# Performance work log

Measured on AMD Instinct MI355X. Metric: run time of the kernel, lower is better.

## Reference

```python
import jax, jax.numpy as jnp
import numpy as np

V = 8192        # num_embeddings == n_nodes
E = 262144      # n_edges (avg degree 32)
N = 262144      # lookup batch
D = 128         # out_channels
LAMDA = 0.8
EPS = 1e-12


def setup_inputs() -> dict:
    key = jax.random.key(0)
    k0, k1, k2, k3, k4 = jax.random.split(key, 5)
    x = jax.random.randint(k0, (N,), 0, V)
    edge_index = jax.random.randint(k1, (2, E), 0, V)
    edge_weight = jax.random.uniform(k2, (E,), dtype=jnp.float32)
    embedding = jax.random.normal(k3, (V, V), dtype=jnp.float32) * 0.02
    W = jax.random.normal(k4, (V, D), dtype=jnp.float32) * (1.0 / np.sqrt(V))
    b = jnp.zeros((D,), dtype=jnp.float32)
    return {"x": x, "edge_index": edge_index, "edge_weight": edge_weight,
            "embedding": embedding, "W": W, "b": b}


def reference(x, edge_index, edge_weight, embedding, W, b):
    # Embedding_sim: linear transform then sparse adjacency propagation
    H = embedding @ W + b                       # [V, D]
    src, dst = edge_index[0], edge_index[1]
    msg = H[src] * edge_weight[:, None]         # gather + weight, [E, D]
    P = jax.ops.segment_sum(msg, dst, num_segments=V)  # spmm(A, H), [V, D]
    emb = LAMDA * P + (1.0 - LAMDA) * H         # [V, D]
    # dropout is identity in eval mode
    out = emb[x]                                # embedding lookup, [N, D]
    norm = jnp.linalg.norm(out, axis=-1, keepdims=True)
    return out / jnp.maximum(norm, EPS)         # F.normalize (L2, dim=1)
```

## Files before the change

kernel.cpp:

```cpp
#include <hip/hip_runtime.h>
#include <hip/hip_bf16.h>

#define V     8192
#define E_N   262144
#define NN    262144
#define D     128
#define KDIM  8192

typedef __attribute__((ext_vector_type(8))) short b16x8;
typedef __attribute__((ext_vector_type(4))) float f32x4;

static __device__ __forceinline__ unsigned short f2bf(float f) {
    union { float f; unsigned int u; } v; v.f = f;
    unsigned int r = v.u + 0x7FFFu + ((v.u >> 16) & 1u);
    return (unsigned short)(r >> 16);
}

static __device__ __forceinline__ unsigned int cvtpk(float lo, float hi) {
    unsigned int r;
    asm("v_cvt_pk_bf16_f32 %0, %1, %2" : "=v"(r) : "v"(lo), "v"(hi));
    return r;
}

__global__ void k_pack(const float* __restrict__ W, unsigned short* __restrict__ Wp) {
    __shared__ float tile[32][129];
    int kb = blockIdx.x;
    int t  = threadIdx.x;
    #pragma unroll
    for (int i = 0; i < 16; i++) {
        int lin = i * 256 + t;
        int kk = lin >> 7, c = lin & 127;
        tile[kk][c] = W[(size_t)(kb * 32 + kk) * D + c];
    }
    __syncthreads();
    unsigned short* outp = Wp + (size_t)kb * 4096;
    #pragma unroll
    for (int i = 0; i < 16; i++) {
        int o = i * 256 + t;
        int c = o >> 5, kk = o & 31;
        outp[o] = f2bf(tile[kk][c]);
    }
}

__global__ void k_initH(float* __restrict__ H, const float* __restrict__ b) {
    int t = blockIdx.x * 256 + threadIdx.x;
    H[t] = b[t & (D - 1)];
}

__global__ void k_hist(const int* __restrict__ dst, int* __restrict__ hist) {
    int e = blockIdx.x * 256 + threadIdx.x;
    if (e < E_N) atomicAdd(&hist[dst[e]], 1);
}

__global__ void k_scan(const int* __restrict__ hist, int* __restrict__ offsets,
                       int* __restrict__ cursor) {
    __shared__ int part[1024];
    int t = threadIdx.x;
    int base = t * 8;
    int loc[8]; int s = 0;
    for (int i = 0; i < 8; i++) { loc[i] = s; s += hist[base + i]; }
    part[t] = s;
    __syncthreads();
    for (int st = 1; st < 1024; st <<= 1) {
        int v = (t >= st) ? part[t - st] : 0;
        __syncthreads();
        part[t] += v;
        __syncthreads();
    }
    int ex = (t == 0) ? 0 : part[t - 1];
    for (int i = 0; i < 8; i++) {
        int o = ex + loc[i];
        offsets[base + i] = o;
        cursor[base + i] = o;
    }
    if (t == 1023) offsets[8192] = ex + s;
}

__global__ void k_scatter(const int* __restrict__ srcI, const int* __restrict__ dstI,
                          const float* __restrict__ w, int* __restrict__ cursor,
                          int* __restrict__ src_s, float* __restrict__ w_s) {
    int e = blockIdx.x * 256 + threadIdx.x;
    if (e < E_N) {
        int dnode = dstI[e];
        int pos = atomicAdd(&cursor[dnode], 1);
        src_s[pos] = srcI[e];
        w_s[pos]  = w[e];
    }
}

__global__ void __launch_bounds__(256) k_gemm(const float* __restrict__ A,
                                              const unsigned short* __restrict__ Wp,
                                              float* __restrict__ H) {
    const int rb   = blockIdx.x >> 3;
    const int ks   = blockIdx.x & 7;
    const int tid  = threadIdx.x;
    const int w    = tid >> 6;
    const int lane = tid & 63;
    const int r16  = lane & 15;
    const int kg   = lane >> 4;

    const float* aP = A + (size_t)(rb * 64 + w * 16 + r16) * KDIM + ks * 1024 + kg * 8;
    const unsigned short* bP = Wp + (size_t)(ks * 32) * 4096 + r16 * 32 + kg * 8;

    f32x4 acc[8];
    f32x4 zero = {0.f, 0.f, 0.f, 0.f};
    #pragma unroll
    for (int t = 0; t < 8; t++) acc[t] = zero;

#define ISSUE(aa0, aa1, bb, kt)                                        \
    do {                                                               \
        const float* ap_ = aP + (kt) * 32;                             \
        aa0 = *(const f32x4*)ap_;                                      \
        aa1 = *(const f32x4*)(ap_ + 4);                                \
        const b16x8* bp_ = (const b16x8*)(bP + (size_t)(kt) * 4096);   \
        _Pragma("unroll")                                              \
        for (int t = 0; t < 8; t++) bb[t] = bp_[t * 64];               \
    } while (0)

#define COMPUTE(aa0, aa1, bb)                                                          \
    do {                                                                               \
        union { b16x8 v; unsigned int u[4]; } af_;                                     \
        af_.u[0] = cvtpk(aa0[0], aa0[1]);                                              \
        af_.u[1] = cvtpk(aa0[2], aa0[3]);                                              \
        af_.u[2] = cvtpk(aa1[0], aa1[1]);                                              \
        af_.u[3] = cvtpk(aa1[2], aa1[3]);                                              \
        _Pragma("unroll")                                                              \
        for (int t = 0; t < 8; t++)                                                    \
            acc[t] = __builtin_amdgcn_mfma_f32_16x16x32_bf16(af_.v, bb[t], acc[t], 0, 0, 0); \
    } while (0)

    f32x4 a0A, a1A, a0B, a1B;
    b16x8 bA[8], bB[8];

    ISSUE(a0A, a1A, bA, 0);
    for (int kt = 0; kt < 32; kt += 2) {
        ISSUE(a0B, a1B, bB, kt + 1);
        COMPUTE(a0A, a1A, bA);
        ISSUE(a0A, a1A, bA, (kt + 2) & 31);
        COMPUTE(a0B, a1B, bB);
    }
#undef ISSUE
#undef COMPUTE

    const int rbase = rb * 64 + w * 16 + kg * 4;
    #pragma unroll
    for (int t = 0; t < 8; t++) {
        int col = t * 16 + r16;
        #pragma unroll
        for (int j = 0; j < 4; j++)
            atomicAdd(&H[(size_t)(rbase + j) * D + col], acc[t][j]);
    }
}

__global__ void k_emb(const float* __restrict__ H, const int* __restrict__ offsets,
                      const int* __restrict__ src_s, const float* __restrict__ w_s,
                      float* __restrict__ embn) {
    __shared__ float red[128];
    int v = blockIdx.x;
    int d = threadIdx.x;
    int s0 = offsets[v], s1 = offsets[v + 1];
    float acc = 0.f;
    for (int i = s0; i < s1; i++) {
        int s = src_s[i];
        float w = w_s[i];
        acc = fmaf(w, H[(size_t)s * D + d], acc);
    }
    float e = 0.8f * acc + 0.2f * H[(size_t)v * D + d];
    red[d] = e * e;
    __syncthreads();
    for (int st = 64; st > 0; st >>= 1) {
        if (d < st) red[d] += red[d + st];
        __syncthreads();
    }
    float norm = sqrtf(red[0]);
    float scale = 1.f / fmaxf(norm, 1e-12f);
    embn[(size_t)v * D + d] = e * scale;
}

__global__ void k_out(const int* __restrict__ x, const float* __restrict__ embn,
                      float* __restrict__ out) {
    int t = blockIdx.x * 256 + threadIdx.x;
    int n = t >> 5, c = t & 31;
    int xv = x[n];
    ((f32x4*)out)[t] = ((const f32x4*)embn)[xv * 32 + c];
}

extern "C" void kernel_launch(void* const* d_in, const int* in_sizes, int n_in,
                              void* d_out, int out_size, void* d_ws, size_t ws_size,
                              hipStream_t stream) {
    const int*   x      = (const int*)d_in[0];
    const int*   eSrc   = (const int*)d_in[1];
    const int*   eDst   = ((const int*)d_in[1]) + E_N;
    const float* eW     = (const float*)d_in[2];
    const float* A      = (const float*)d_in[3];
    const float* W      = (const float*)d_in[4];
    const float* b      = (const float*)d_in[5];
    float* out = (float*)d_out;

    char* ws = (char*)d_ws;
    unsigned short* Wp  = (unsigned short*)(ws);
    float* H            = (float*)(ws + (2u << 20));
    float* embn         = (float*)(ws + (6u << 20));
    int* offsets        = (int*)(ws + (10u << 20));
    int* cursor         = (int*)(ws + (10u << 20) + 40960);
    int* src_s          = (int*)(ws + (10u << 20) + 131072);
    float* w_s          = (float*)(ws + (10u << 20) + 131072 + (1u << 20));

    hipMemsetAsync(cursor, 0, V * sizeof(int), stream);
    k_pack   <<<256, 256, 0, stream>>>(W, Wp);
    k_initH  <<<(V * D) / 256, 256, 0, stream>>>(H, b);
    k_hist   <<<E_N / 256, 256, 0, stream>>>(eDst, cursor);
    k_scan   <<<1, 1024, 0, stream>>>(cursor, offsets, cursor);
    k_scatter<<<E_N / 256, 256, 0, stream>>>(eSrc, eDst, eW, cursor, src_s, w_s);
    k_gemm   <<<1024, 256, 0, stream>>>(A, Wp, H);
    k_emb    <<<V, D, 0, stream>>>(H, offsets, src_s, w_s, embn);
    k_out    <<<(NN * 32) / 256, 256, 0, stream>>>(x, embn, out);
}
```

Baseline: 227.3 us.

## Replace split-K atomics with partial buffers and deepen GEMM prefetch pipeline

The GEMM now splits K four ways instead of eight, uses 512 blocks, and writes each split's partial results to its own buffer instead of doing float atomicAdd into H. A new combine kernel sums the four partials and adds the bias, which also removes the separate bias-init kernel. The cursor memset is folded into the pack kernel, and the GEMM main loop keeps four A stages and two B stages in flight with a launch-bounds occupancy hint. This trades global atomic traffic and two launches for extra partial-buffer memory traffic, one extra launch, and fewer blocks to hide latency.

```diff
diff --git a/kernel.cpp b/kernel.cpp
--- a/kernel.cpp
+++ b/kernel.cpp
@@ -22,10 +22,12 @@
     return r;
 }
 
-__global__ void k_pack(const float* __restrict__ W, unsigned short* __restrict__ Wp) {
+__global__ void k_pack(const float* __restrict__ W, unsigned short* __restrict__ Wp,
+                       int* __restrict__ cursor) {
     __shared__ float tile[32][129];
     int kb = blockIdx.x;
     int t  = threadIdx.x;
+    if (kb < 32) cursor[kb * 256 + t] = 0;
     #pragma unroll
     for (int i = 0; i < 16; i++) {
         int lin = i * 256 + t;
@@ -40,11 +42,6 @@
         int c = o >> 5, kk = o & 31;
         outp[o] = f2bf(tile[kk][c]);
     }
-}
-
-__global__ void k_initH(float* __restrict__ H, const float* __restrict__ b) {
-    int t = blockIdx.x * 256 + threadIdx.x;
-    H[t] = b[t & (D - 1)];
 }
 
 __global__ void k_hist(const int* __restrict__ dst, int* __restrict__ hist) {
@@ -88,68 +85,81 @@
     }
 }
 
-__global__ void __launch_bounds__(256) k_gemm(const float* __restrict__ A,
-                                              const unsigned short* __restrict__ Wp,
-                                              float* __restrict__ H) {
-    const int rb   = blockIdx.x >> 3;
-    const int ks   = blockIdx.x & 7;
+__global__ void __launch_bounds__(256, 2) k_gemm(const float* __restrict__ A,
+                                                 const unsigned short* __restrict__ Wp,
+                                                 float* __restrict__ Hp) {
+    const int rb   = blockIdx.x >> 2;
+    const int ks   = blockIdx.x & 3;
     const int tid  = threadIdx.x;
     const int w    = tid >> 6;
     const int lane = tid & 63;
     const int r16  = lane & 15;
     const int kg   = lane >> 4;
 
-    const float* aP = A + (size_t)(rb * 64 + w * 16 + r16) * KDIM + ks * 1024 + kg * 8;
-    const unsigned short* bP = Wp + (size_t)(ks * 32) * 4096 + r16 * 32 + kg * 8;
+    const float* aP = A + (size_t)(rb * 64 + w * 16 + r16) * KDIM + ks * 2048 + kg * 8;
+    const unsigned short* bP = Wp + (size_t)(ks * 64) * 4096 + r16 * 32 + kg * 8;
 
     f32x4 acc[8];
     f32x4 zero = {0.f, 0.f, 0.f, 0.f};
     #pragma unroll
     for (int t = 0; t < 8; t++) acc[t] = zero;
 
-#define ISSUE(aa0, aa1, bb, kt)                                        \
-    do {                                                               \
-        const float* ap_ = aP + (kt) * 32;                             \
-        aa0 = *(const f32x4*)ap_;                                      \
-        aa1 = *(const f32x4*)(ap_ + 4);                                \
-        const b16x8* bp_ = (const b16x8*)(bP + (size_t)(kt) * 4096);   \
-        _Pragma("unroll")                                              \
-        for (int t = 0; t < 8; t++) bb[t] = bp_[t * 64];               \
+#define LDA(s0, s1, p)                                                  \
+    do { const float* ap_ = aP + (size_t)(p) * 32;                      \
+         s0 = *(const f32x4*)ap_; s1 = *(const f32x4*)(ap_ + 4); } while (0)
+#define LDB(bb, p)                                                      \
+    do { const b16x8* bp_ = (const b16x8*)(bP + (size_t)(p) * 4096);    \
+         _Pragma("unroll")                                              \
+         for (int t = 0; t < 8; t++) bb[t] = bp_[t * 64]; } while (0)
+#define COMP(s0, s1, bb)                                                \
+    do { union { b16x8 v; unsigned int u[4]; } af_;                     \
+         af_.u[0] = cvtpk(s0[0], s0[1]);                                \
+         af_.u[1] = cvtpk(s0[2], s0[3]);                                \
+         af_.u[2] = cvtpk(s1[0], s1[1]);                                \
+         af_.u[3] = cvtpk(s1[2], s1[3]);                                \
+         _Pragma("unroll")                                              \
+         for (int t = 0; t < 8; t++)                                    \
+             acc[t] = __builtin_amdgcn_mfma_f32_16x16x32_bf16(af_.v, bb[t], acc[t], 0, 0, 0); \
     } while (0)
-
-#define COMPUTE(aa0, aa1, bb)                                                          \
-    do {                                                                               \
-        union { b16x8 v; unsigned int u[4]; } af_;                                     \
-        af_.u[0] = cvtpk(aa0[0], aa0[1]);                                              \
-        af_.u[1] = cvtpk(aa0[2], aa0[3]);                                              \
-        af_.u[2] = cvtpk(aa1[0], aa1[1]);                                              \
-        af_.u[3] = cvtpk(aa1[2], aa1[3]);                                              \
-        _Pragma("unroll")                                                              \
-        for (int t = 0; t < 8; t++)                                                    \
-            acc[t] = __builtin_amdgcn_mfma_f32_16x16x32_bf16(af_.v, bb[t], acc[t], 0, 0, 0); \
-    } while (0)
-
-    f32x4 a0A, a1A, a0B, a1B;
-    b16x8 bA[8], bB[8];
-
-    ISSUE(a0A, a1A, bA, 0);
-    for (int kt = 0; kt < 32; kt += 2) {
-        ISSUE(a0B, a1B, bB, kt + 1);
-        COMPUTE(a0A, a1A, bA);
-        ISSUE(a0A, a1A, bA, (kt + 2) & 31);
-        COMPUTE(a0B, a1B, bB);
-    }
-#undef ISSUE
-#undef COMPUTE
-
-    const int rbase = rb * 64 + w * 16 + kg * 4;
-    #pragma unroll
-    for (int t = 0; t < 8; t++) {
-        int col = t * 16 + r16;
+#define CL(p) ((p) < 64 ? (p) : 63)
+
+    f32x4 a00, a01, a10, a11, a20, a21, a30, a31;
+    b16x8 b0[8], b1[8];
+
+    LDA(a00, a01, 0);
+    LDA(a10, a11, 1);
+    LDB(b0, 0);
+    LDA(a20, a21, 2);
+    LDB(b1, 1);
+    LDA(a30, a31, 3);
+
+    for (int p = 0; p < 64; p += 4) {
+        COMP(a00, a01, b0); LDB(b0, CL(p + 2)); LDA(a00, a01, CL(p + 4));
+        COMP(a10, a11, b1); LDB(b1, CL(p + 3)); LDA(a10, a11, CL(p + 5));
+        COMP(a20, a21, b0); LDB(b0, CL(p + 4)); LDA(a20, a21, CL(p + 6));
+        COMP(a30, a31, b1); LDB(b1, CL(p + 5)); LDA(a30, a31, CL(p + 7));
+    }
+#undef LDA
+#undef LDB
+#undef COMP
+#undef CL
+
+    float* hp = Hp + ((size_t)ks * V + (size_t)(rb * 64 + w * 16 + kg * 4)) * D + r16;
+    #pragma unroll
+    for (int t = 0; t < 8; t++)
         #pragma unroll
         for (int j = 0; j < 4; j++)
-            atomicAdd(&H[(size_t)(rbase + j) * D + col], acc[t][j]);
-    }
+            hp[(size_t)j * D + t * 16] = acc[t][j];
+}
+
+__global__ void k_comb(const float* __restrict__ Hp, const float* __restrict__ b,
+                       float* __restrict__ H) {
+    int i = blockIdx.x * 256 + threadIdx.x;
+    f32x4 bb = *(const f32x4*)(b + (i & 31) * 4);
+    const f32x4* hp = (const f32x4*)Hp;
+    const size_t q = (size_t)V * D / 4;
+    f32x4 s = bb + hp[i] + hp[i + q] + hp[i + 2 * q] + hp[i + 3 * q];
+    ((f32x4*)H)[i] = s;
 }
 
 __global__ void k_emb(const float* __restrict__ H, const int* __restrict__ offsets,
@@ -201,18 +211,18 @@
     unsigned short* Wp  = (unsigned short*)(ws);
     float* H            = (float*)(ws + (2u << 20));
     float* embn         = (float*)(ws + (6u << 20));
-    int* offsets        = (int*)(ws + (10u << 20));
-    int* cursor         = (int*)(ws + (10u << 20) + 40960);
-    int* src_s          = (int*)(ws + (10u << 20) + 131072);
-    float* w_s          = (float*)(ws + (10u << 20) + 131072 + (1u << 20));
-
-    hipMemsetAsync(cursor, 0, V * sizeof(int), stream);
-    k_pack   <<<256, 256, 0, stream>>>(W, Wp);
-    k_initH  <<<(V * D) / 256, 256, 0, stream>>>(H, b);
+    float* Hp           = (float*)(ws + (10u << 20));
+    int* offsets        = (int*)(ws + (26u << 20));
+    int* cursor         = (int*)(ws + (26u << 20) + 40960);
+    int* src_s          = (int*)(ws + (26u << 20) + 131072);
+    float* w_s          = (float*)(ws + (26u << 20) + 131072 + (1u << 20));
+
+    k_pack   <<<256, 256, 0, stream>>>(W, Wp, cursor);
     k_hist   <<<E_N / 256, 256, 0, stream>>>(eDst, cursor);
     k_scan   <<<1, 1024, 0, stream>>>(cursor, offsets, cursor);
     k_scatter<<<E_N / 256, 256, 0, stream>>>(eSrc, eDst, eW, cursor, src_s, w_s);
-    k_gemm   <<<1024, 256, 0, stream>>>(A, Wp, H);
+    k_gemm   <<<512, 256, 0, stream>>>(A, Wp, Hp);
+    k_comb   <<<(V * D / 4) / 256, 256, 0, stream>>>(Hp, b, H);
     k_emb    <<<V, D, 0, stream>>>(H, offsets, src_s, w_s, embn);
     k_out    <<<(NN * 32) / 256, 256, 0, stream>>>(x, embn, out);
 }
```

Measured after the change: 219.6 us. 1.04x faster.
